# Kernel optimization log

Hardware: AMD Instinct MI355X
Metric: run time of the kernel (lower is better)

## Reference

```python
import jax, jax.numpy as jnp
import numpy as np
import math

B, S, D, H = 4, 2048, 512, 8
HD = D // H  # head dim = 64

def setup_inputs() -> dict:
    key = jax.random.key(0)
    ks = jax.random.split(key, 12)
    inp = {
        'queries': jax.random.normal(ks[0], (B, S, D), jnp.float32),
        'keys': jax.random.normal(ks[1], (B, S, D), jnp.float32),
        'values': jax.random.normal(ks[2], (B, S, D), jnp.float32),
        'valid_lens': jax.random.randint(ks[3], (B,), 0, 2048, jnp.int32),
        'Wq': jax.random.normal(ks[4], (D, D), jnp.float32) / math.sqrt(D),
        'bq': jnp.zeros((D,), jnp.float32),
        'Wk': jax.random.normal(ks[5], (D, D), jnp.float32) / math.sqrt(D),
        'bk': jnp.zeros((D,), jnp.float32),
        'Wv': jax.random.normal(ks[6], (D, D), jnp.float32) / math.sqrt(D),
        'bv': jnp.zeros((D,), jnp.float32),
        'Wo': jax.random.normal(ks[7], (D, D), jnp.float32) / math.sqrt(D),
        'bo': jnp.zeros((D,), jnp.float32),
    }
    return inp

def reference(queries, keys, values, valid_lens, Wq, bq, Wk, bk, Wv, bv, Wo, bo):
    # project and split heads: [B,S,D] -> [B,H,S,HD]
    def split_heads(x):
        return x.reshape(B, S, H, HD).transpose(0, 2, 1, 3)
    q = split_heads(queries @ Wq + bq)
    k = split_heads(keys @ Wk + bk)
    v = split_heads(values @ Wv + bv)
    # scores [B,H,Sq,Sk]
    scores = jnp.einsum('bhqd,bhkd->bhqk', q, k) / math.sqrt(HD)
    # masked softmax: mask key positions >= valid_len with -1e6 (d2l semantics)
    mask = jnp.arange(S)[None, None, None, :] < valid_lens[:, None, None, None]
    scores = jnp.where(mask, scores, -1e6)
    attn = jax.nn.softmax(scores, axis=-1)
    out = jnp.einsum('bhqk,bhkd->bhqd', attn, v)  # [B,H,S,HD]
    out = out.transpose(0, 2, 1, 3).reshape(B, S, D)
    return out @ Wo + bo
```

## Files before the change

kernel.cpp:

```cpp
#include <hip/hip_runtime.h>
#include <hip/hip_bf16.h>

typedef _Float16 half8 __attribute__((ext_vector_type(8)));
typedef _Float16 half4 __attribute__((ext_vector_type(4)));
typedef _Float16 half2t __attribute__((ext_vector_type(2)));
typedef float floatx4 __attribute__((ext_vector_type(4)));
typedef float floatx16 __attribute__((ext_vector_type(16)));
typedef unsigned int uint2v __attribute__((ext_vector_type(2)));

#define LOG2E 1.44269504088896340736f

__device__ __forceinline__ half8 cvt8r(floatx4 a, floatx4 b) {
    half8 h;
    h[0] = (_Float16)a[0]; h[1] = (_Float16)a[1]; h[2] = (_Float16)a[2]; h[3] = (_Float16)a[3];
    h[4] = (_Float16)b[0]; h[5] = (_Float16)b[1]; h[6] = (_Float16)b[2]; h[7] = (_Float16)b[3];
    return h;
}

union H8U { half8 h; half2t v2[4]; uint2v u[2]; };

__device__ __forceinline__ half2t pk16(float a, float b) {
    return __builtin_bit_cast(half2t, __builtin_amdgcn_cvt_pkrtz(a, b));
}

__global__ __launch_bounds__(256) void transpose_w_kernel(
        const float* __restrict__ Wq, const float* __restrict__ Wk,
        const float* __restrict__ Wv, const float* __restrict__ Wo,
        _Float16* __restrict__ out) {
    const float* W = (blockIdx.z == 0) ? Wq : (blockIdx.z == 1) ? Wk : (blockIdx.z == 2) ? Wv : Wo;
    _Float16* o = out + (size_t)blockIdx.z * 512 * 512;
    __shared__ __align__(16) _Float16 t[64][72];
    int r0 = blockIdx.x * 64, c0 = blockIdx.y * 64;
    int tid = threadIdx.x;
    for (int i = 0; i < 2; i++) {
        int f = i * 256 + tid;
        int row = f >> 3, seg = f & 7;
        const float* p = W + (size_t)(r0 + row) * 512 + c0 + seg * 8;
        *(half8*)&t[row][seg * 8] = cvt8r(*(const floatx4*)p, *(const floatx4*)(p + 4));
    }
    __syncthreads();
    for (int i = 0; i < 2; i++) {
        int f = i * 256 + tid;
        int crow = f >> 3, seg = f & 7;
        half8 hv;
        for (int j = 0; j < 8; j++) hv[j] = t[seg * 8 + j][crow];
        *(half8*)(o + (size_t)(c0 + crow) * 512 + r0 + seg * 8) = hv;
    }
}

__global__ __launch_bounds__(256) void gemm_qkv_kernel(
        const float* __restrict__ Xq, const float* __restrict__ Xk, const float* __restrict__ Xv,
        const _Float16* __restrict__ WTall,
        const float* __restrict__ bq, const float* __restrict__ bk, const float* __restrict__ bv,
        const int* __restrict__ vlens,
        _Float16* __restrict__ qo, _Float16* __restrict__ ko2, _Float16* __restrict__ vto) {
    int z = blockIdx.z;
    int mBase = blockIdx.x * 64, nBase = blockIdx.y * 128;

    if (z >= 1) {
        int b_ = mBase >> 11, s0 = mBase & 2047;
        int L = vlens[b_];
        if (s0 >= L && !(z == 2 && L == 0)) return;
    }

    const float* X = (z == 0) ? Xq : (z == 1) ? Xk : Xv;
    const _Float16* BT = WTall + (size_t)z * 512 * 512;
    const float* bias = (z == 0) ? bq : (z == 1) ? bk : bv;

    __shared__ __align__(16) _Float16 Asm[64][72];
    __shared__ __align__(16) _Float16 Bsm[128][72];

    int tid = threadIdx.x;
    int wave = tid >> 6, lane = tid & 63;
    int lrow = lane & 15, quad = lane >> 4;
    int mrow = wave * 16 + lrow;

    const floatx4 fz = {0.f, 0.f, 0.f, 0.f};
    floatx4 acc[8];
    for (int i = 0; i < 8; i++) acc[i] = fz;

    int arow[2], aseg[2], brow[4], bseg[4];
    for (int i = 0; i < 2; i++) { int f = i * 256 + tid; arow[i] = f >> 3; aseg[i] = f & 7; }
    for (int i = 0; i < 4; i++) { int f = i * 256 + tid; brow[i] = f >> 3; bseg[i] = f & 7; }

    floatx4 areg[2][2];
    half8 breg[4];
    for (int i = 0; i < 2; i++) {
        const float* pa = X + (size_t)(mBase + arow[i]) * 512 + aseg[i] * 8;
        areg[i][0] = *(const floatx4*)pa;
        areg[i][1] = *(const floatx4*)(pa + 4);
    }
    for (int i = 0; i < 4; i++)
        breg[i] = *(const half8*)(BT + (size_t)(nBase + brow[i]) * 512 + bseg[i] * 8);

    for (int kb = 0; kb < 512; kb += 64) {
        for (int i = 0; i < 2; i++) *(half8*)&Asm[arow[i]][aseg[i] * 8] = cvt8r(areg[i][0], areg[i][1]);
        for (int i = 0; i < 4; i++) *(half8*)&Bsm[brow[i]][bseg[i] * 8] = breg[i];
        __syncthreads();
        if (kb + 64 < 512) {
            int kn = kb + 64;
            for (int i = 0; i < 2; i++) {
                const float* pa = X + (size_t)(mBase + arow[i]) * 512 + kn + aseg[i] * 8;
                areg[i][0] = *(const floatx4*)pa;
                areg[i][1] = *(const floatx4*)(pa + 4);
            }
            for (int i = 0; i < 4; i++)
                breg[i] = *(const half8*)(BT + (size_t)(nBase + brow[i]) * 512 + kn + bseg[i] * 8);
        }
        for (int kc = 0; kc < 2; kc++) {
            int ko_ = kc * 32 + quad * 8;
            half8 a = *(const half8*)&Asm[mrow][ko_];
            for (int nt = 0; nt < 8; nt++) {
                half8 b = *(const half8*)&Bsm[nt * 16 + lrow][ko_];
                acc[nt] = __builtin_amdgcn_mfma_f32_16x16x32_f16(a, b, acc[nt], 0, 0, 0);
            }
        }
        __syncthreads();
    }

    if (z == 2) {
        for (int nt = 0; nt < 8; nt++) {
            int gc = nBase + nt * 16 + lrow;
            float bb = bias[gc];
            int h = gc >> 6, hd = gc & 63;
            int gr = mBase + wave * 16 + quad * 4;
            int b_ = gr >> 11, s = gr & 2047;
            half4 hv;
            for (int r = 0; r < 4; r++) hv[r] = (_Float16)(acc[nt][r] + bb);
            *(half4*)(vto + (((size_t)(b_ * 8 + h) * 64 + hd) * 2048 + s)) = hv;
        }
    } else {
        _Float16* out = (z == 0) ? qo : ko2;
        for (int nt = 0; nt < 8; nt++) {
            int gc = nBase + nt * 16 + lrow;
            float bb = bias[gc];
            int h = gc >> 6, hd = gc & 63;
            for (int r = 0; r < 4; r++) {
                int gr = mBase + wave * 16 + quad * 4 + r;
                int b_ = gr >> 11, s = gr & 2047;
                out[(((size_t)b_ * 8 + h) * 2048 + s) * 64 + hd] = (_Float16)(acc[nt][r] + bb);
            }
        }
    }
}

__global__ __launch_bounds__(128) void attn_kernel(
        const _Float16* __restrict__ qws, const _Float16* __restrict__ kws,
        const _Float16* __restrict__ vtws, const int* __restrict__ vlens,
        _Float16* __restrict__ aout) {
    int idx = blockIdx.x;
    int b = ((idx & 3) + (idx >> 8)) & 3;
    int h = (idx >> 2) & 7;
    int q0 = ((idx >> 5) & 31) * 64;
    int bh = b * 8 + h;
    int L = vlens[b];
    bool uni = (L == 0);
    int nkt = uni ? 16 : ((L + 127) >> 7);
    int nfull = uni ? 0 : (L >> 7);

    int tid = threadIdx.x;
    int wq = tid >> 6;
    int lane = tid & 63;
    int l31 = lane & 31, hi = lane >> 5;

    __shared__ __align__(16) _Float16 ksm[128 * 64];
    __shared__ __align__(16) _Float16 vtsm[64 * 128];
    char* ksmB = (char*)ksm;
    char* vsmB = (char*)vtsm;

    const _Float16* kbase = kws + (size_t)bh * 2048 * 64;
    const _Float16* vtbase = vtws + (size_t)bh * 64 * 2048;

    half8 qf[4];
    {
        const _Float16* qrow = qws + ((size_t)bh * 2048 + q0 + wq * 32 + l31) * 64;
#pragma unroll
        for (int kc = 0; kc < 4; kc++) {
            qf[kc] = *(const half8*)(qrow + kc * 16 + hi * 8);
            qf[kc] = qf[kc] * (_Float16)(0.125f * LOG2E);
        }
    }

    floatx16 oc0, oc1;
#pragma unroll
    for (int i = 0; i < 16; i++) { oc0[i] = 0.f; oc1[i] = 0.f; }
    float rsp0 = 0.f, rsp1 = 0.f;

    int kthr = tid >> 3, ksg = tid & 7;
    int vthr = tid >> 4, vsg = tid & 15;
    int x15 = l31 & 15, x7 = l31 & 7;

    half8 kreg[8], vreg[8];
#pragma unroll
    for (int i = 0; i < 8; i++) {
        kreg[i] = *(const half8*)(kbase + (i * 16 + kthr) * 64 + ksg * 8);
        vreg[i] = *(const half8*)(vtbase + (size_t)(i * 8 + vthr) * 2048 + vsg * 8);
    }

    for (int kt = 0; kt < nkt; kt++) {
#pragma unroll
        for (int i = 0; i < 8; i++) {
            int kr = i * 16 + kthr;
            *(half8*)(ksmB + kr * 128 + ((ksg ^ (kr & 7)) << 4)) = kreg[i];
            int vr = i * 8 + vthr;
            *(half8*)(vsmB + vr * 256 + ((vsg ^ (vr & 15)) << 4)) = vreg[i];
        }
        __syncthreads();
        if (kt + 1 < nkt) {
            const _Float16* kn = kbase + (size_t)(kt + 1) * 128 * 64;
            const _Float16* vn = vtbase + (kt + 1) * 128;
#pragma unroll
            for (int i = 0; i < 8; i++) {
                kreg[i] = *(const half8*)(kn + (i * 16 + kthr) * 64 + ksg * 8);
                vreg[i] = *(const half8*)(vn + (size_t)(i * 8 + vthr) * 2048 + vsg * 8);
            }
        }

#pragma unroll
        for (int t = 0; t < 4; t++) {
            if (!uni && kt * 128 + t * 32 >= L) continue;

            floatx16 sacc;
#pragma unroll
            for (int i = 0; i < 16; i++) sacc[i] = 0.f;
            int rbase = (t * 32 + l31) * 128;
#pragma unroll
            for (int kc = 0; kc < 4; kc++) {
                int c = 2 * kc + hi;
                half8 kf = *(const half8*)(ksmB + rbase + ((c ^ x7) << 4));
                sacc = __builtin_amdgcn_mfma_f32_32x32x16_f16(kf, qf[kc], sacc, 0, 0, 0);
            }

            float p[16];
            if (kt < nfull) {
#pragma unroll
                for (int r = 0; r < 16; r++) p[r] = exp2f(sacc[r]);
            } else {
                int kb0 = kt * 128 + t * 32 + 4 * hi;
#pragma unroll
                for (int r = 0; r < 16; r++) {
                    int key = kb0 + (r & 3) + 8 * (r >> 2);
                    p[r] = uni ? 1.0f : ((key < L) ? exp2f(sacc[r]) : 0.0f);
                }
            }
            float ts = (((p[0] + p[1]) + (p[2] + p[3])) + ((p[4] + p[5]) + (p[6] + p[7])))
                     + (((p[8] + p[9]) + (p[10] + p[11])) + ((p[12] + p[13]) + (p[14] + p[15])));
            if (t & 1) rsp1 += ts; else rsp0 += ts;

#pragma unroll
            for (int s2 = 0; s2 < 2; s2++) {
                int s = t * 2 + s2;
                H8U pa;
#pragma unroll
                for (int jj = 0; jj < 4; jj++)
                    pa.v2[jj] = pk16(p[s2 * 8 + jj * 2], p[s2 * 8 + jj * 2 + 1]);
                int cA = (((2 * s) ^ x15) << 4) + 8 * hi;
                int cB = (((2 * s + 1) ^ x15) << 4) + 8 * hi;
                int ro0 = l31 * 256, ro1 = (32 + l31) * 256;
                H8U vf0, vf1;
                vf0.u[0] = *(const uint2v*)(vsmB + ro0 + cA);
                vf0.u[1] = *(const uint2v*)(vsmB + ro0 + cB);
                vf1.u[0] = *(const uint2v*)(vsmB + ro1 + cA);
                vf1.u[1] = *(const uint2v*)(vsmB + ro1 + cB);
                oc0 = __builtin_amdgcn_mfma_f32_32x32x16_f16(pa.h, vf0.h, oc0, 0, 0, 0);
                oc1 = __builtin_amdgcn_mfma_f32_32x32x16_f16(pa.h, vf1.h, oc1, 0, 0, 0);
            }
        }
        __syncthreads();
    }

    float rs = rsp0 + rsp1;
    float rstot = rs + __shfl_xor(rs, 32, 64);
    _Float16* outb = aout + ((size_t)b * 2048 + q0 + wq * 32) * 512 + h * 64;
#pragma unroll
    for (int r = 0; r < 16; r++) {
        int qi = (r & 3) + 8 * (r >> 2) + 4 * hi;
        float inv = 1.0f / __shfl(rstot, qi, 64);
        outb[(size_t)qi * 512 + l31] = (_Float16)(oc0[r] * inv);
        outb[(size_t)qi * 512 + 32 + l31] = (_Float16)(oc1[r] * inv);
    }
}

__global__ __launch_bounds__(256) void gemm_out_kernel(
        const _Float16* __restrict__ A, const _Float16* __restrict__ BT,
        const float* __restrict__ bias, float* __restrict__ out) {
    __shared__ __align__(16) _Float16 Asm[64][72];
    __shared__ __align__(16) _Float16 Bsm[128][72];

    int tid = threadIdx.x;
    int wave = tid >> 6, lane = tid & 63;
    int lrow = lane & 15, quad = lane >> 4;
    int mBase = blockIdx.x * 64, nBase = blockIdx.y * 128;
    int mrow = wave * 16 + lrow;

    const floatx4 fz = {0.f, 0.f, 0.f, 0.f};
    floatx4 acc[8];
    for (int i = 0; i < 8; i++) acc[i] = fz;

    int arow[2], aseg[2], brow[4], bseg[4];
    for (int i = 0; i < 2; i++) { int f = i * 256 + tid; arow[i] = f >> 3; aseg[i] = f & 7; }
    for (int i = 0; i < 4; i++) { int f = i * 256 + tid; brow[i] = f >> 3; bseg[i] = f & 7; }

    half8 areg[2], breg[4];
    for (int i = 0; i < 2; i++)
        areg[i] = *(const half8*)(A + (size_t)(mBase + arow[i]) * 512 + aseg[i] * 8);
    for (int i = 0; i < 4; i++)
        breg[i] = *(const half8*)(BT + (size_t)(nBase + brow[i]) * 512 + bseg[i] * 8);

    for (int kb = 0; kb < 512; kb += 64) {
        for (int i = 0; i < 2; i++) *(half8*)&Asm[arow[i]][aseg[i] * 8] = areg[i];
        for (int i = 0; i < 4; i++) *(half8*)&Bsm[brow[i]][bseg[i] * 8] = breg[i];
        __syncthreads();
        if (kb + 64 < 512) {
            int kn = kb + 64;
            for (int i = 0; i < 2; i++)
                areg[i] = *(const half8*)(A + (size_t)(mBase + arow[i]) * 512 + kn + aseg[i] * 8);
            for (int i = 0; i < 4; i++)
                breg[i] = *(const half8*)(BT + (size_t)(nBase + brow[i]) * 512 + kn + bseg[i] * 8);
        }
        for (int kc = 0; kc < 2; kc++) {
            int ko_ = kc * 32 + quad * 8;
            half8 a = *(const half8*)&Asm[mrow][ko_];
            for (int nt = 0; nt < 8; nt++) {
                half8 b = *(const half8*)&Bsm[nt * 16 + lrow][ko_];
                acc[nt] = __builtin_amdgcn_mfma_f32_16x16x32_f16(a, b, acc[nt], 0, 0, 0);
            }
        }
        __syncthreads();
    }

    for (int nt = 0; nt < 8; nt++) {
        int gc = nBase + nt * 16 + lrow;
        float bb = bias[gc];
        for (int r = 0; r < 4; r++) {
            int gr = mBase + wave * 16 + quad * 4 + r;
            out[(size_t)gr * 512 + gc] = acc[nt][r] + bb;
        }
    }
}

extern "C" void kernel_launch(void* const* d_in, const int* in_sizes, int n_in,
                              void* d_out, int out_size, void* d_ws, size_t ws_size,
                              hipStream_t stream) {
    const float* Q  = (const float*)d_in[0];
    const float* K  = (const float*)d_in[1];
    const float* V  = (const float*)d_in[2];
    const int*   VL = (const int*)d_in[3];
    const float* Wq = (const float*)d_in[4];
    const float* bq = (const float*)d_in[5];
    const float* Wk = (const float*)d_in[6];
    const float* bk = (const float*)d_in[7];
    const float* Wv = (const float*)d_in[8];
    const float* bv = (const float*)d_in[9];
    const float* Wo = (const float*)d_in[10];
    const float* bo = (const float*)d_in[11];

    char* ws = (char*)d_ws;
    _Float16* WT   = (_Float16*)ws;
    _Float16* qws  = (_Float16*)(ws + (size_t)(2)  * 1024 * 1024);
    _Float16* kws  = (_Float16*)(ws + (size_t)(10) * 1024 * 1024);
    _Float16* aout = (_Float16*)(ws + (size_t)(18) * 1024 * 1024);
    _Float16* vtws = (_Float16*)(ws + (size_t)(26) * 1024 * 1024);

    transpose_w_kernel<<<dim3(8, 8, 4), 256, 0, stream>>>(Wq, Wk, Wv, Wo, WT);
    gemm_qkv_kernel<<<dim3(128, 4, 3), 256, 0, stream>>>(Q, K, V, WT, bq, bk, bv, VL, qws, kws, vtws);
    attn_kernel<<<dim3(1024, 1, 1), 128, 0, stream>>>(qws, kws, vtws, VL, aout);
    gemm_out_kernel<<<dim3(128, 4, 1), 256, 0, stream>>>(aout, WT + (size_t)3 * 512 * 512, bo, (float*)d_out);
}
```

Measured before the change: 195.4 us.

## Split attention across four key-range partitions with a separate combine kernel

The attention kernel now splits each (batch, head, query-block) job into four key-range splits, flash-decoding style, launching four times as many blocks with 64-key tiles and smaller shared memory. Each split writes a normalized partial output and its row sum to workspace. A new combine kernel reweights the partials by their row sums and writes the final attention output. The goal is more parallelism and occupancy, since per-batch valid lengths are uneven and the earlier grid had long serial key loops. The cost is an extra kernel launch and extra global traffic for the partials, and each split re-loads Q.

```diff
diff --git a/kernel.cpp b/kernel.cpp
--- a/kernel.cpp
+++ b/kernel.cpp
@@ -144,27 +144,35 @@
     }
 }
 
-__global__ __launch_bounds__(128) void attn_kernel(
+__global__ __launch_bounds__(128, 4) void attn_kernel(
         const _Float16* __restrict__ qws, const _Float16* __restrict__ kws,
         const _Float16* __restrict__ vtws, const int* __restrict__ vlens,
-        _Float16* __restrict__ aout) {
+        _Float16* __restrict__ pOh, float* __restrict__ prs) {
     int idx = blockIdx.x;
-    int b = ((idx & 3) + (idx >> 8)) & 3;
-    int h = (idx >> 2) & 7;
-    int q0 = ((idx >> 5) & 31) * 64;
+    int s_ = idx & 3;
+    int bhq = idx >> 2;
+    int b = ((bhq & 3) + (bhq >> 8)) & 3;
+    int h = (bhq >> 2) & 7;
+    int qb = (bhq >> 5) & 31;
+    int q0 = qb * 64;
     int bh = b * 8 + h;
+    int slot = ((bh * 32 + qb) << 2) | s_;
     int L = vlens[b];
     bool uni = (L == 0);
-    int nkt = uni ? 16 : ((L + 127) >> 7);
-    int nfull = uni ? 0 : (L >> 7);
+    int nkt = uni ? 32 : ((L + 63) >> 6);
+    int nfull = uni ? 0 : (L >> 6);
+    int quota = (nkt + 3) >> 2;
+    int kt0 = s_ * quota;
+    int kt1 = min(kt0 + quota, nkt);
 
     int tid = threadIdx.x;
     int wq = tid >> 6;
     int lane = tid & 63;
     int l31 = lane & 31, hi = lane >> 5;
-
-    __shared__ __align__(16) _Float16 ksm[128 * 64];
-    __shared__ __align__(16) _Float16 vtsm[64 * 128];
+    int x7 = l31 & 7;
+
+    __shared__ __align__(16) _Float16 ksm[64 * 64];
+    __shared__ __align__(16) _Float16 vtsm[64 * 64];
     char* ksmB = (char*)ksm;
     char* vsmB = (char*)vtsm;
 
@@ -184,41 +192,45 @@
     floatx16 oc0, oc1;
 #pragma unroll
     for (int i = 0; i < 16; i++) { oc0[i] = 0.f; oc1[i] = 0.f; }
-    float rsp0 = 0.f, rsp1 = 0.f;
-
-    int kthr = tid >> 3, ksg = tid & 7;
-    int vthr = tid >> 4, vsg = tid & 15;
-    int x15 = l31 & 15, x7 = l31 & 7;
-
-    half8 kreg[8], vreg[8];
-#pragma unroll
-    for (int i = 0; i < 8; i++) {
-        kreg[i] = *(const half8*)(kbase + (i * 16 + kthr) * 64 + ksg * 8);
-        vreg[i] = *(const half8*)(vtbase + (size_t)(i * 8 + vthr) * 2048 + vsg * 8);
-    }
-
-    for (int kt = 0; kt < nkt; kt++) {
-#pragma unroll
-        for (int i = 0; i < 8; i++) {
-            int kr = i * 16 + kthr;
-            *(half8*)(ksmB + kr * 128 + ((ksg ^ (kr & 7)) << 4)) = kreg[i];
-            int vr = i * 8 + vthr;
-            *(half8*)(vsmB + vr * 256 + ((vsg ^ (vr & 15)) << 4)) = vreg[i];
-        }
-        __syncthreads();
-        if (kt + 1 < nkt) {
-            const _Float16* kn = kbase + (size_t)(kt + 1) * 128 * 64;
-            const _Float16* vn = vtbase + (kt + 1) * 128;
-#pragma unroll
-            for (int i = 0; i < 8; i++) {
-                kreg[i] = *(const half8*)(kn + (i * 16 + kthr) * 64 + ksg * 8);
-                vreg[i] = *(const half8*)(vn + (size_t)(i * 8 + vthr) * 2048 + vsg * 8);
-            }
-        }
-
-#pragma unroll
-        for (int t = 0; t < 4; t++) {
-            if (!uni && kt * 128 + t * 32 >= L) continue;
+    float rs = 0.f;
+
+    int thr = tid >> 3, sg = tid & 7;
+
+    half8 kreg[4], vreg[4];
+    if (kt0 < kt1) {
+        const _Float16* kp = kbase + (size_t)kt0 * 64 * 64;
+        const _Float16* vp = vtbase + kt0 * 64;
+#pragma unroll
+        for (int i = 0; i < 4; i++) {
+            int row = i * 16 + thr;
+            kreg[i] = *(const half8*)(kp + row * 64 + sg * 8);
+            vreg[i] = *(const half8*)(vp + (size_t)row * 2048 + sg * 8);
+        }
+    }
+
+    for (int kt = kt0; kt < kt1; kt++) {
+#pragma unroll
+        for (int i = 0; i < 4; i++) {
+            int row = i * 16 + thr;
+            int wo = row * 128 + ((sg ^ (row & 7)) << 4);
+            *(half8*)(ksmB + wo) = kreg[i];
+            *(half8*)(vsmB + wo) = vreg[i];
+        }
+        __syncthreads();
+        if (kt + 1 < kt1) {
+            const _Float16* kp = kbase + (size_t)(kt + 1) * 64 * 64;
+            const _Float16* vp = vtbase + (kt + 1) * 64;
+#pragma unroll
+            for (int i = 0; i < 4; i++) {
+                int row = i * 16 + thr;
+                kreg[i] = *(const half8*)(kp + row * 64 + sg * 8);
+                vreg[i] = *(const half8*)(vp + (size_t)row * 2048 + sg * 8);
+            }
+        }
+
+#pragma unroll
+        for (int t = 0; t < 2; t++) {
+            if (!uni && kt * 64 + t * 32 >= L) continue;
 
             floatx16 sacc;
 #pragma unroll
@@ -226,8 +238,7 @@
             int rbase = (t * 32 + l31) * 128;
 #pragma unroll
             for (int kc = 0; kc < 4; kc++) {
-                int c = 2 * kc + hi;
-                half8 kf = *(const half8*)(ksmB + rbase + ((c ^ x7) << 4));
+                half8 kf = *(const half8*)(ksmB + rbase + (((2 * kc + hi) ^ x7) << 4));
                 sacc = __builtin_amdgcn_mfma_f32_32x32x16_f16(kf, qf[kc], sacc, 0, 0, 0);
             }
 
@@ -236,16 +247,15 @@
 #pragma unroll
                 for (int r = 0; r < 16; r++) p[r] = exp2f(sacc[r]);
             } else {
-                int kb0 = kt * 128 + t * 32 + 4 * hi;
+                int kb0 = kt * 64 + t * 32 + 4 * hi;
 #pragma unroll
                 for (int r = 0; r < 16; r++) {
                     int key = kb0 + (r & 3) + 8 * (r >> 2);
                     p[r] = uni ? 1.0f : ((key < L) ? exp2f(sacc[r]) : 0.0f);
                 }
             }
-            float ts = (((p[0] + p[1]) + (p[2] + p[3])) + ((p[4] + p[5]) + (p[6] + p[7])))
-                     + (((p[8] + p[9]) + (p[10] + p[11])) + ((p[12] + p[13]) + (p[14] + p[15])));
-            if (t & 1) rsp1 += ts; else rsp0 += ts;
+            rs += (((p[0] + p[1]) + (p[2] + p[3])) + ((p[4] + p[5]) + (p[6] + p[7])))
+                + (((p[8] + p[9]) + (p[10] + p[11])) + ((p[12] + p[13]) + (p[14] + p[15])));
 
 #pragma unroll
             for (int s2 = 0; s2 < 2; s2++) {
@@ -254,14 +264,13 @@
 #pragma unroll
                 for (int jj = 0; jj < 4; jj++)
                     pa.v2[jj] = pk16(p[s2 * 8 + jj * 2], p[s2 * 8 + jj * 2 + 1]);
-                int cA = (((2 * s) ^ x15) << 4) + 8 * hi;
-                int cB = (((2 * s + 1) ^ x15) << 4) + 8 * hi;
-                int ro0 = l31 * 256, ro1 = (32 + l31) * 256;
+                int offA = (((2 * s) ^ x7) << 4) + 8 * hi;
+                int ro0 = l31 * 128, ro1 = (32 + l31) * 128;
                 H8U vf0, vf1;
-                vf0.u[0] = *(const uint2v*)(vsmB + ro0 + cA);
-                vf0.u[1] = *(const uint2v*)(vsmB + ro0 + cB);
-                vf1.u[0] = *(const uint2v*)(vsmB + ro1 + cA);
-                vf1.u[1] = *(const uint2v*)(vsmB + ro1 + cB);
+                vf0.u[0] = *(const uint2v*)(vsmB + ro0 + offA);
+                vf0.u[1] = *(const uint2v*)(vsmB + ro0 + (offA ^ 16));
+                vf1.u[0] = *(const uint2v*)(vsmB + ro1 + offA);
+                vf1.u[1] = *(const uint2v*)(vsmB + ro1 + (offA ^ 16));
                 oc0 = __builtin_amdgcn_mfma_f32_32x32x16_f16(pa.h, vf0.h, oc0, 0, 0, 0);
                 oc1 = __builtin_amdgcn_mfma_f32_32x32x16_f16(pa.h, vf1.h, oc1, 0, 0, 0);
             }
@@ -269,16 +278,57 @@
         __syncthreads();
     }
 
-    float rs = rsp0 + rsp1;
     float rstot = rs + __shfl_xor(rs, 32, 64);
-    _Float16* outb = aout + ((size_t)b * 2048 + q0 + wq * 32) * 512 + h * 64;
+    float myinv = (rstot > 0.f) ? (1.f / rstot) : 0.f;
+    if (hi == 0) prs[(size_t)slot * 64 + wq * 32 + l31] = rstot;
+
+    _Float16* po = pOh + (size_t)slot * 4096 + (size_t)wq * 32 * 64;
 #pragma unroll
     for (int r = 0; r < 16; r++) {
         int qi = (r & 3) + 8 * (r >> 2) + 4 * hi;
-        float inv = 1.0f / __shfl(rstot, qi, 64);
-        outb[(size_t)qi * 512 + l31] = (_Float16)(oc0[r] * inv);
-        outb[(size_t)qi * 512 + 32 + l31] = (_Float16)(oc1[r] * inv);
-    }
+        float w = __shfl(myinv, qi, 64);
+        po[(size_t)qi * 64 + l31] = (_Float16)(oc0[r] * w);
+        po[(size_t)qi * 64 + 32 + l31] = (_Float16)(oc1[r] * w);
+    }
+}
+
+__global__ __launch_bounds__(256) void combine_kernel(
+        const _Float16* __restrict__ pOh, const float* __restrict__ prs,
+        _Float16* __restrict__ aout) {
+    int bq = blockIdx.x;
+    int bh = bq >> 5, qb = bq & 31;
+    int b = bh >> 3, h = bh & 7;
+    int slot0 = bq << 2;
+    int tid = threadIdx.x;
+    int q = tid >> 2, c0 = (tid & 3) * 16;
+
+    float r0 = prs[(size_t)(slot0 + 0) * 64 + q];
+    float r1 = prs[(size_t)(slot0 + 1) * 64 + q];
+    float r2 = prs[(size_t)(slot0 + 2) * 64 + q];
+    float r3 = prs[(size_t)(slot0 + 3) * 64 + q];
+    float invt = 1.f / (r0 + r1 + r2 + r3);
+    float w[4] = {r0 * invt, r1 * invt, r2 * invt, r3 * invt};
+
+    float acc[16];
+#pragma unroll
+    for (int e = 0; e < 16; e++) acc[e] = 0.f;
+#pragma unroll
+    for (int s = 0; s < 4; s++) {
+        const _Float16* p = pOh + (size_t)(slot0 + s) * 4096 + (size_t)q * 64 + c0;
+        half8 a = *(const half8*)p;
+        half8 bvec = *(const half8*)(p + 8);
+#pragma unroll
+        for (int e = 0; e < 8; e++) {
+            acc[e] += w[s] * (float)a[e];
+            acc[8 + e] += w[s] * (float)bvec[e];
+        }
+    }
+    half8 o0, o1;
+#pragma unroll
+    for (int e = 0; e < 8; e++) { o0[e] = (_Float16)acc[e]; o1[e] = (_Float16)acc[8 + e]; }
+    _Float16* op = aout + ((size_t)b * 2048 + qb * 64 + q) * 512 + h * 64 + c0;
+    *(half8*)op = o0;
+    *(half8*)(op + 8) = o1;
 }
 
 __global__ __launch_bounds__(256) void gemm_out_kernel(
@@ -361,9 +411,12 @@
     _Float16* kws  = (_Float16*)(ws + (size_t)(10) * 1024 * 1024);
     _Float16* aout = (_Float16*)(ws + (size_t)(18) * 1024 * 1024);
     _Float16* vtws = (_Float16*)(ws + (size_t)(26) * 1024 * 1024);
+    _Float16* pOh  = (_Float16*)(ws + (size_t)(34) * 1024 * 1024);
+    float*    prs  = (float*)   (ws + (size_t)(66) * 1024 * 1024);
 
     transpose_w_kernel<<<dim3(8, 8, 4), 256, 0, stream>>>(Wq, Wk, Wv, Wo, WT);
     gemm_qkv_kernel<<<dim3(128, 4, 3), 256, 0, stream>>>(Q, K, V, WT, bq, bk, bv, VL, qws, kws, vtws);
-    attn_kernel<<<dim3(1024, 1, 1), 128, 0, stream>>>(qws, kws, vtws, VL, aout);
+    attn_kernel<<<dim3(4096, 1, 1), 128, 0, stream>>>(qws, kws, vtws, VL, pOh, prs);
+    combine_kernel<<<dim3(1024, 1, 1), 256, 0, stream>>>(pOh, prs, aout);
     gemm_out_kernel<<<dim3(128, 4, 1), 256, 0, stream>>>(aout, WT + (size_t)3 * 512 * 512, bo, (float*)d_out);
 }
```

Measured after the change: 212.2 us. +8.6%, slower.

## Load K/V fragments directly from global memory in single-wave attention blocks

Applied to the files above, without the earlier changes.

The attention kernel changes from two-wave blocks that stage 128-key K and V^T tiles through swizzled LDS with barriers into one-wave blocks of 32 queries. Each block loads its MFMA K and V fragments straight from global memory in 64-key steps, and the grid doubles to 2048 blocks with a new block-index mapping. This removes LDS traffic, barriers and the register-prefetch staging, and gives more, smaller blocks for occupancy. In exchange, K/V reuse across waves is lost, so each K/V tile is fetched by twice as many blocks, with less explicit latency hiding.

```diff
diff --git a/kernel.cpp b/kernel.cpp
--- a/kernel.cpp
+++ b/kernel.cpp
@@ -144,36 +144,33 @@
     }
 }
 
-__global__ __launch_bounds__(128) void attn_kernel(
+__global__ __launch_bounds__(64) void attn_kernel(
         const _Float16* __restrict__ qws, const _Float16* __restrict__ kws,
         const _Float16* __restrict__ vtws, const int* __restrict__ vlens,
         _Float16* __restrict__ aout) {
     int idx = blockIdx.x;
-    int b = ((idx & 3) + (idx >> 8)) & 3;
-    int h = (idx >> 2) & 7;
-    int q0 = ((idx >> 5) & 31) * 64;
+    int h = idx & 7;
+    int j = idx >> 3;
+    int b = j & 3;
+    int q0 = (j >> 2) * 32;
     int bh = b * 8 + h;
     int L = vlens[b];
     bool uni = (L == 0);
-    int nkt = uni ? 16 : ((L + 127) >> 7);
-    int nfull = uni ? 0 : (L >> 7);
-
-    int tid = threadIdx.x;
-    int wq = tid >> 6;
-    int lane = tid & 63;
+    int nkt = uni ? 32 : ((L + 63) >> 6);
+    int nfull = uni ? 0 : (L >> 6);
+
+    int lane = threadIdx.x;
     int l31 = lane & 31, hi = lane >> 5;
 
-    __shared__ __align__(16) _Float16 ksm[128 * 64];
-    __shared__ __align__(16) _Float16 vtsm[64 * 128];
-    char* ksmB = (char*)ksm;
-    char* vsmB = (char*)vtsm;
-
-    const _Float16* kbase = kws + (size_t)bh * 2048 * 64;
-    const _Float16* vtbase = vtws + (size_t)bh * 64 * 2048;
+    const _Float16* kb = kws + (size_t)bh * 2048 * 64;
+    const _Float16* vb = vtws + (size_t)bh * 64 * 2048;
+    const _Float16* vrow0 = vb + (size_t)l31 * 2048;
+    const _Float16* vrow1 = vb + (size_t)(32 + l31) * 2048;
+    const _Float16* krow = kb + (size_t)l31 * 64 + hi * 8;
 
     half8 qf[4];
     {
-        const _Float16* qrow = qws + ((size_t)bh * 2048 + q0 + wq * 32 + l31) * 64;
+        const _Float16* qrow = qws + ((size_t)bh * 2048 + q0 + l31) * 64;
 #pragma unroll
         for (int kc = 0; kc < 4; kc++) {
             qf[kc] = *(const half8*)(qrow + kc * 16 + hi * 8);
@@ -184,100 +181,76 @@
     floatx16 oc0, oc1;
 #pragma unroll
     for (int i = 0; i < 16; i++) { oc0[i] = 0.f; oc1[i] = 0.f; }
-    float rsp0 = 0.f, rsp1 = 0.f;
-
-    int kthr = tid >> 3, ksg = tid & 7;
-    int vthr = tid >> 4, vsg = tid & 15;
-    int x15 = l31 & 15, x7 = l31 & 7;
-
-    half8 kreg[8], vreg[8];
-#pragma unroll
-    for (int i = 0; i < 8; i++) {
-        kreg[i] = *(const half8*)(kbase + (i * 16 + kthr) * 64 + ksg * 8);
-        vreg[i] = *(const half8*)(vtbase + (size_t)(i * 8 + vthr) * 2048 + vsg * 8);
-    }
+    float rs = 0.f;
 
     for (int kt = 0; kt < nkt; kt++) {
-#pragma unroll
-        for (int i = 0; i < 8; i++) {
-            int kr = i * 16 + kthr;
-            *(half8*)(ksmB + kr * 128 + ((ksg ^ (kr & 7)) << 4)) = kreg[i];
-            int vr = i * 8 + vthr;
-            *(half8*)(vsmB + vr * 256 + ((vsg ^ (vr & 15)) << 4)) = vreg[i];
-        }
-        __syncthreads();
-        if (kt + 1 < nkt) {
-            const _Float16* kn = kbase + (size_t)(kt + 1) * 128 * 64;
-            const _Float16* vn = vtbase + (kt + 1) * 128;
-#pragma unroll
-            for (int i = 0; i < 8; i++) {
-                kreg[i] = *(const half8*)(kn + (i * 16 + kthr) * 64 + ksg * 8);
-                vreg[i] = *(const half8*)(vn + (size_t)(i * 8 + vthr) * 2048 + vsg * 8);
-            }
-        }
-
-#pragma unroll
-        for (int t = 0; t < 4; t++) {
-            if (!uni && kt * 128 + t * 32 >= L) continue;
+        int kk = kt * 64;
+        int ng = uni ? 2 : ((L - kk >= 33) ? 2 : 1);
+
+        half8 kf[2][4];
+        H8U vf[2][2][2];
+#pragma unroll
+        for (int t = 0; t < 2; t++) {
+#pragma unroll
+            for (int kc = 0; kc < 4; kc++)
+                kf[t][kc] = *(const half8*)(krow + (size_t)(kk + t * 32) * 64 + kc * 16);
+#pragma unroll
+            for (int s2 = 0; s2 < 2; s2++) {
+                int col = kk + (t * 2 + s2) * 16 + 4 * hi;
+                vf[t][s2][0].u[0] = *(const uint2v*)(vrow0 + col);
+                vf[t][s2][0].u[1] = *(const uint2v*)(vrow0 + col + 8);
+                vf[t][s2][1].u[0] = *(const uint2v*)(vrow1 + col);
+                vf[t][s2][1].u[1] = *(const uint2v*)(vrow1 + col + 8);
+            }
+        }
+
+#pragma unroll
+        for (int t = 0; t < 2; t++) {
+            if (t >= ng) break;
 
             floatx16 sacc;
 #pragma unroll
             for (int i = 0; i < 16; i++) sacc[i] = 0.f;
-            int rbase = (t * 32 + l31) * 128;
-#pragma unroll
-            for (int kc = 0; kc < 4; kc++) {
-                int c = 2 * kc + hi;
-                half8 kf = *(const half8*)(ksmB + rbase + ((c ^ x7) << 4));
-                sacc = __builtin_amdgcn_mfma_f32_32x32x16_f16(kf, qf[kc], sacc, 0, 0, 0);
-            }
+#pragma unroll
+            for (int kc = 0; kc < 4; kc++)
+                sacc = __builtin_amdgcn_mfma_f32_32x32x16_f16(kf[t][kc], qf[kc], sacc, 0, 0, 0);
 
             float p[16];
             if (kt < nfull) {
 #pragma unroll
                 for (int r = 0; r < 16; r++) p[r] = exp2f(sacc[r]);
             } else {
-                int kb0 = kt * 128 + t * 32 + 4 * hi;
+                int kb0 = kk + t * 32 + 4 * hi;
 #pragma unroll
                 for (int r = 0; r < 16; r++) {
                     int key = kb0 + (r & 3) + 8 * (r >> 2);
                     p[r] = uni ? 1.0f : ((key < L) ? exp2f(sacc[r]) : 0.0f);
                 }
             }
-            float ts = (((p[0] + p[1]) + (p[2] + p[3])) + ((p[4] + p[5]) + (p[6] + p[7])))
-                     + (((p[8] + p[9]) + (p[10] + p[11])) + ((p[12] + p[13]) + (p[14] + p[15])));
-            if (t & 1) rsp1 += ts; else rsp0 += ts;
+            rs += (((p[0] + p[1]) + (p[2] + p[3])) + ((p[4] + p[5]) + (p[6] + p[7])))
+                + (((p[8] + p[9]) + (p[10] + p[11])) + ((p[12] + p[13]) + (p[14] + p[15])));
 
 #pragma unroll
             for (int s2 = 0; s2 < 2; s2++) {
-                int s = t * 2 + s2;
                 H8U pa;
 #pragma unroll
                 for (int jj = 0; jj < 4; jj++)
                     pa.v2[jj] = pk16(p[s2 * 8 + jj * 2], p[s2 * 8 + jj * 2 + 1]);
-                int cA = (((2 * s) ^ x15) << 4) + 8 * hi;
-                int cB = (((2 * s + 1) ^ x15) << 4) + 8 * hi;
-                int ro0 = l31 * 256, ro1 = (32 + l31) * 256;
-                H8U vf0, vf1;
-                vf0.u[0] = *(const uint2v*)(vsmB + ro0 + cA);
-                vf0.u[1] = *(const uint2v*)(vsmB + ro0 + cB);
-                vf1.u[0] = *(const uint2v*)(vsmB + ro1 + cA);
-                vf1.u[1] = *(const uint2v*)(vsmB + ro1 + cB);
-                oc0 = __builtin_amdgcn_mfma_f32_32x32x16_f16(pa.h, vf0.h, oc0, 0, 0, 0);
-                oc1 = __builtin_amdgcn_mfma_f32_32x32x16_f16(pa.h, vf1.h, oc1, 0, 0, 0);
-            }
-        }
-        __syncthreads();
-    }
-
-    float rs = rsp0 + rsp1;
+                oc0 = __builtin_amdgcn_mfma_f32_32x32x16_f16(pa.h, vf[t][s2][0].h, oc0, 0, 0, 0);
+                oc1 = __builtin_amdgcn_mfma_f32_32x32x16_f16(pa.h, vf[t][s2][1].h, oc1, 0, 0, 0);
+            }
+        }
+    }
+
     float rstot = rs + __shfl_xor(rs, 32, 64);
-    _Float16* outb = aout + ((size_t)b * 2048 + q0 + wq * 32) * 512 + h * 64;
+    float myinv = 1.0f / rstot;
+    _Float16* outb = aout + ((size_t)b * 2048 + q0) * 512 + h * 64;
 #pragma unroll
     for (int r = 0; r < 16; r++) {
         int qi = (r & 3) + 8 * (r >> 2) + 4 * hi;
-        float inv = 1.0f / __shfl(rstot, qi, 64);
-        outb[(size_t)qi * 512 + l31] = (_Float16)(oc0[r] * inv);
-        outb[(size_t)qi * 512 + 32 + l31] = (_Float16)(oc1[r] * inv);
+        float w = __shfl(myinv, qi, 64);
+        outb[(size_t)qi * 512 + l31] = (_Float16)(oc0[r] * w);
+        outb[(size_t)qi * 512 + 32 + l31] = (_Float16)(oc1[r] * w);
     }
 }
 
@@ -364,6 +337,6 @@
 
     transpose_w_kernel<<<dim3(8, 8, 4), 256, 0, stream>>>(Wq, Wk, Wv, Wo, WT);
     gemm_qkv_kernel<<<dim3(128, 4, 3), 256, 0, stream>>>(Q, K, V, WT, bq, bk, bv, VL, qws, kws, vtws);
-    attn_kernel<<<dim3(1024, 1, 1), 128, 0, stream>>>(qws, kws, vtws, VL, aout);
+    attn_kernel<<<dim3(2048, 1, 1), 64, 0, stream>>>(qws, kws, vtws, VL, aout);
     gemm_out_kernel<<<dim3(128, 4, 1), 256, 0, stream>>>(aout, WT + (size_t)3 * 512 * 512, bo, (float*)d_out);
 }
```

After: 278.7 us. +42.6%, slower.
